# Kernel optimization log

Hardware: AMD Instinct MI355X
Metric: run time of the kernel (lower is better)

The kernel has to match this reference:

```python
import jax, jax.numpy as jnp
import numpy as np

N = 8000          # num_nodes
DEG = 8           # avg out-degree of random road graph
B = 32            # batch size
INPUT_DIM = 2
UNITS = 64        # rnn_units
K = 2             # max_diffusion_step
NUM_SUPPORTS = 2  # dual_random_walk


def _spmm(rows, cols, vals, x):
    # sparse @ dense: y[r] += vals * x[c] for each coo entry (r, c)
    return jax.ops.segment_sum(vals[:, None] * x[cols], rows, num_segments=N)


def _gconv(inputs, state, supports, W, b):
    # Chebyshev-style diffusion conv, faithful to GCONV.forward layout
    Bsz = inputs.shape[0]
    x = jnp.concatenate([inputs.reshape(Bsz, N, -1), state.reshape(Bsz, N, -1)], axis=2)
    F = x.shape[2]                                   # input_dim + units
    x0 = jnp.transpose(x, (1, 2, 0)).reshape(N, F * Bsz)
    xs = [x0]
    for rows, cols, vals in supports:
        x1 = _spmm(rows, cols, vals, x0)
        xs.append(x1)
        xk2, xk1 = x0, x1
        for _ in range(2, K + 1):
            x2 = 2.0 * _spmm(rows, cols, vals, xk1) - xk2
            xs.append(x2)
            xk2, xk1 = xk1, x2
    M = len(xs)                                      # num_matrices = 2*K+1
    xc = jnp.stack(xs).reshape(M, N, F, Bsz)
    xc = jnp.transpose(xc, (3, 1, 2, 0)).reshape(Bsz * N, F * M)
    out = xc @ W + b
    return out.reshape(Bsz, N * W.shape[1])


def setup_inputs() -> dict:
    rng = np.random.default_rng(0)
    rows = np.repeat(np.arange(N, dtype=np.int32), DEG)
    cols = rng.integers(0, N, size=N * DEG).astype(np.int32)
    vals = rng.uniform(0.5, 1.5, size=N * DEG).astype(np.float32)
    # random-walk normalization: rw(A) = D^-1 A ; supports are rw(A).T and rw(A.T).T
    rsum = np.zeros(N, np.float32); np.add.at(rsum, rows, vals)
    csum = np.zeros(N, np.float32); np.add.at(csum, cols, vals)
    rinv = np.where(rsum > 0, 1.0 / np.maximum(rsum, 1e-12), 0.0).astype(np.float32)
    cinv = np.where(csum > 0, 1.0 / np.maximum(csum, 1e-12), 0.0).astype(np.float32)
    # support0 = (D^-1 A)^T: entry (cols[i], rows[i]) = vals[i] * rinv[rows[i]]
    s0_rows, s0_cols, s0_vals = cols, rows, (vals * rinv[rows]).astype(np.float32)
    # support1 = (D_T^-1 A^T)^T: entry (rows[i], cols[i]) = vals[i] * cinv[cols[i]]
    s1_rows, s1_cols, s1_vals = rows, cols, (vals * cinv[cols]).astype(np.float32)

    key = jax.random.key(0)
    k1, k2, k3, k4 = jax.random.split(key, 4)
    F = INPUT_DIM + UNITS
    M = NUM_SUPPORTS * K + 1
    xavier = lambda k, shape: jax.random.normal(k, shape, jnp.float32) * np.float32(np.sqrt(2.0 / (shape[0] + shape[1])))
    W_ru = xavier(k1, (F * M, 2 * UNITS))
    b_ru = jnp.ones((2 * UNITS,), jnp.float32)    # bias_start=1.0
    W_c = xavier(k2, (F * M, UNITS))
    b_c = jnp.zeros((UNITS,), jnp.float32)        # bias_start=0.0
    inputs = jax.random.normal(k3, (B, N * INPUT_DIM), jnp.float32)
    hx = jax.random.normal(k4, (B, N * UNITS), jnp.float32)
    return {
        "inputs": inputs, "hx": hx,
        "W_ru": W_ru, "b_ru": b_ru, "W_c": W_c, "b_c": b_c,
        "s0_rows": jnp.asarray(s0_rows), "s0_cols": jnp.asarray(s0_cols), "s0_vals": jnp.asarray(s0_vals),
        "s1_rows": jnp.asarray(s1_rows), "s1_cols": jnp.asarray(s1_cols), "s1_vals": jnp.asarray(s1_vals),
    }


def reference(inputs, hx, W_ru, b_ru, W_c, b_c,
              s0_rows, s0_cols, s0_vals, s1_rows, s1_cols, s1_vals):
    supports = [(s0_rows, s0_cols, s0_vals), (s1_rows, s1_cols, s1_vals)]
    value = jax.nn.sigmoid(_gconv(inputs, hx, supports, W_ru, b_ru))
    value = value.reshape(-1, N, 2 * UNITS)
    r = value[..., :UNITS].reshape(-1, N * UNITS)
    u = value[..., UNITS:].reshape(-1, N * UNITS)
    c = jnp.tanh(_gconv(inputs, r * hx, supports, W_c, b_c))
    return u * hx + (1.0 - u) * c
```

## Files before the change

### kernel.cpp

```cpp
#include <hip/hip_runtime.h>
#include <stdint.h>

typedef unsigned short u16;
typedef unsigned int   u32;

typedef __attribute__((ext_vector_type(8))) short bf16x8;
typedef __attribute__((ext_vector_type(4))) float f32x4;

#define NNODES 8000
#define BSZ    32
#define UNITS  64
#define EDG    64000
#define ROWCH  288
#define ROWU16 2304
#define KLIN   480
#define HXROW  512000
#define INROW  16000
#define NROW   18432000
#define NSTEPS 15

__device__ __forceinline__ u32 f2bf(float f){
    u32 u = __float_as_uint(f);
    return (u + 0x7FFFu + ((u >> 16) & 1u)) >> 16;
}
__device__ __forceinline__ float bfu(u16 s){ return __uint_as_float(((u32)s) << 16); }
__device__ __forceinline__ float lo16(u32 u){ return __uint_as_float(u << 16); }
__device__ __forceinline__ float hi16(u32 u){ return __uint_as_float(u & 0xFFFF0000u); }
__device__ __forceinline__ float sigm(float x){ return 1.f / (1.f + __expf(-x)); }

#define GLDS(gsrc, ldst) \
    __builtin_amdgcn_global_load_lds((const __attribute__((address_space(1))) void*)(gsrc), \
                                     (__attribute__((address_space(3))) void*)(ldst), 16, 0, 0)

__global__ void hist_k(const int* __restrict__ rows, int* __restrict__ counts){
    int e = blockIdx.x * 256 + threadIdx.x;
    if (e < EDG) atomicAdd(&counts[rows[e]], 1);
}

__global__ __launch_bounds__(256) void scan_k(const int* __restrict__ counts,
                                              int* __restrict__ row_ptr,
                                              int* __restrict__ cursor){
    __shared__ int part[256];
    int t = threadIdx.x;
    int s = 0;
    for (int i = 0; i < 32; ++i){ int r = t*32 + i; if (r < NNODES) s += counts[r]; }
    part[t] = s;
    __syncthreads();
    if (t == 0){
        int run = 0;
        for (int i = 0; i < 256; ++i){ int v = part[i]; part[i] = run; run += v; }
    }
    __syncthreads();
    int run = part[t];
    for (int i = 0; i < 32; ++i){
        int r = t*32 + i;
        if (r < NNODES){ row_ptr[r] = run; cursor[r] = run; run += counts[r]; }
    }
    if (t == 255) row_ptr[NNODES] = run;
}

__global__ void scatter_k(const int* __restrict__ rows, const int* __restrict__ cols,
                          const float* __restrict__ vals, int* __restrict__ cursor,
                          int* __restrict__ cs, float* __restrict__ vs){
    int e = blockIdx.x * 256 + threadIdx.x;
    if (e < EDG){
        int r = rows[e];
        int slot = atomicAdd(&cursor[r], 1);
        cs[slot] = cols[e];
        vs[slot] = vals[e];
    }
}

__global__ void prep_w_k(const float* __restrict__ W_ru, const float* __restrict__ W_c,
                         u16* __restrict__ Wt_ru, u16* __restrict__ Wt_c){
    int id = blockIdx.x * 256 + threadIdx.x;
    if (id < 128*KLIN){
        int j = id & 7;
        int cell = id >> 3;
        int col = cell & 127;
        int sq = cell >> 7;
        int kl = sq*8 + j;
        int m = kl / 96, fp = kl - m*96;
        u16 v = 0;
        if (fp < 66){
            float w;
            if (m == 0)      w = W_ru[(fp*5 + 0)*128 + col] - W_ru[(fp*5 + 2)*128 + col] - W_ru[(fp*5 + 4)*128 + col];
            else if (m == 2) w = 2.f * W_ru[(fp*5 + 2)*128 + col];
            else if (m == 4) w = 2.f * W_ru[(fp*5 + 4)*128 + col];
            else             w = W_ru[(fp*5 + m)*128 + col];
            v = (u16)f2bf(w);
        }
        Wt_ru[id] = v;
    }
    int id2 = id - 128*KLIN;
    if (id2 >= 0 && id2 < 64*KLIN){
        int j = id2 & 7;
        int cell = id2 >> 3;
        int col = cell & 63;
        int sq = cell >> 6;
        int kl = sq*8 + j;
        int m = kl / 96, fp = kl - m*96;
        u16 v = 0;
        if (fp < 66){
            float w;
            if (m == 0)      w = W_c[(fp*5 + 0)*64 + col] - W_c[(fp*5 + 2)*64 + col] - W_c[(fp*5 + 4)*64 + col];
            else if (m == 2) w = 2.f * W_c[(fp*5 + 2)*64 + col];
            else if (m == 4) w = 2.f * W_c[(fp*5 + 4)*64 + col];
            else             w = W_c[(fp*5 + m)*64 + col];
            v = (u16)f2bf(w);
        }
        Wt_c[id2] = v;
    }
}

__global__ __launch_bounds__(256) void build_x0_k(const float* __restrict__ inputs,
                                                  const float* __restrict__ hx,
                                                  u16* __restrict__ X0){
    __shared__ float sl[32*72];
    int n = blockIdx.x, t = threadIdx.x;
    #pragma unroll
    for (int i = 0; i < 8; ++i){
        int idx = t + i*256;
        int b = idx >> 6, f = idx & 63;
        sl[b*72 + 2 + f] = hx[b*HXROW + n*64 + f];
    }
    if (t < 64){
        int b = t >> 1, d = t & 1;
        sl[b*72 + d] = inputs[b*INROW + n*2 + d];
    }
    if (t < 192){
        int b = t / 6, k = t - b*6;
        sl[b*72 + 66 + k] = 0.f;
    }
    __syncthreads();
    #pragma unroll
    for (int i = 0; i < 2; ++i){
        int j = t + i*256;
        if (j < ROWCH){
            int b = j & 31, s = j >> 5;
            const float* p = &sl[b*72 + s*8];
            uint4 o;
            o.x = f2bf(p[0]) | (f2bf(p[1]) << 16);
            o.y = f2bf(p[2]) | (f2bf(p[3]) << 16);
            o.z = f2bf(p[4]) | (f2bf(p[5]) << 16);
            o.w = f2bf(p[6]) | (f2bf(p[7]) << 16);
            ((uint4*)X0)[n*ROWCH + j] = o;
        }
    }
}

__device__ __forceinline__ void acc8(float* a, uint4 q, float v){
    a[0] += v*lo16(q.x); a[1] += v*hi16(q.x);
    a[2] += v*lo16(q.y); a[3] += v*hi16(q.y);
    a[4] += v*lo16(q.z); a[5] += v*hi16(q.z);
    a[6] += v*lo16(q.w); a[7] += v*hi16(q.w);
}
__device__ __forceinline__ uint4 pack8(const float* a){
    uint4 o;
    o.x = f2bf(a[0]) | (f2bf(a[1]) << 16);
    o.y = f2bf(a[2]) | (f2bf(a[3]) << 16);
    o.z = f2bf(a[4]) | (f2bf(a[5]) << 16);
    o.w = f2bf(a[6]) | (f2bf(a[7]) << 16);
    return o;
}

__global__ __launch_bounds__(288) void diff1_k(const u16* __restrict__ X0,
                                               u16* __restrict__ X1a, u16* __restrict__ X1b,
                                               const int* __restrict__ rp,
                                               const int* __restrict__ c0, const float* __restrict__ v0,
                                               const int* __restrict__ c1, const float* __restrict__ v1){
    int t = threadIdx.x;
    if (t >= ROWCH) return;
    int n = blockIdx.x;
    const uint4* xb = (const uint4*)X0;
    float a[8] = {0,0,0,0,0,0,0,0};
    float d[8] = {0,0,0,0,0,0,0,0};
    {
        uint4 q[8]; float vv[8];
        #pragma unroll
        for (int i = 0; i < 8; ++i){
            int c = c1[n*8 + i]; vv[i] = v1[n*8 + i];
            q[i] = xb[(size_t)c*ROWCH + t];
        }
        #pragma unroll
        for (int i = 0; i < 8; ++i) acc8(d, q[i], vv[i]);
    }
    int e = rp[n], end = rp[n+1];
    for (; e + 8 <= end; e += 8){
        uint4 q[8]; float vv[8];
        #pragma unroll
        for (int i = 0; i < 8; ++i){
            int c = c0[e+i]; vv[i] = v0[e+i];
            q[i] = xb[(size_t)c*ROWCH + t];
        }
        #pragma unroll
        for (int i = 0; i < 8; ++i) acc8(a, q[i], vv[i]);
    }
    for (; e < end; ++e){
        int c = c0[e]; float v = v0[e];
        acc8(a, xb[(size_t)c*ROWCH + t], v);
    }
    ((uint4*)X1a)[(size_t)n*ROWCH + t] = pack8(a);
    ((uint4*)X1b)[(size_t)n*ROWCH + t] = pack8(d);
}

__global__ __launch_bounds__(288) void diff2_k(const u16* __restrict__ X1a, const u16* __restrict__ X1b,
                                               u16* __restrict__ Y2a, u16* __restrict__ Y2b,
                                               const int* __restrict__ rp,
                                               const int* __restrict__ c0, const float* __restrict__ v0,
                                               const int* __restrict__ c1, const float* __restrict__ v1){
    int t = threadIdx.x;
    if (t >= ROWCH) return;
    int n = blockIdx.x;
    const uint4* xa = (const uint4*)X1a;
    const uint4* xbb = (const uint4*)X1b;
    float a[8] = {0,0,0,0,0,0,0,0};
    float d[8] = {0,0,0,0,0,0,0,0};
    {
        uint4 q[8]; float vv[8];
        #pragma unroll
        for (int i = 0; i < 8; ++i){
            int c = c1[n*8 + i]; vv[i] = v1[n*8 + i];
            q[i] = xbb[(size_t)c*ROWCH + t];
        }
        #pragma unroll
        for (int i = 0; i < 8; ++i) acc8(d, q[i], vv[i]);
    }
    int e = rp[n], end = rp[n+1];
    for (; e + 8 <= end; e += 8){
        uint4 q[8]; float vv[8];
        #pragma unroll
        for (int i = 0; i < 8; ++i){
            int c = c0[e+i]; vv[i] = v0[e+i];
            q[i] = xa[(size_t)c*ROWCH + t];
        }
        #pragma unroll
        for (int i = 0; i < 8; ++i) acc8(a, q[i], vv[i]);
    }
    for (; e < end; ++e){
        int c = c0[e]; float v = v0[e];
        acc8(a, xa[(size_t)c*ROWCH + t], v);
    }
    ((uint4*)Y2a)[(size_t)n*ROWCH + t] = pack8(a);
    ((uint4*)Y2b)[(size_t)n*ROWCH + t] = pack8(d);
}

__global__ __launch_bounds__(512) void gemm_ru_k(
        const u16* X0, const u16* __restrict__ X1a, const u16* __restrict__ X2a,
        const u16* __restrict__ X1b, const u16* __restrict__ X2b,
        const u16* __restrict__ WtS,
        const float* __restrict__ b_ru,
        u16* __restrict__ U, u16* X0st){
    __shared__ u16 Bs[2][4096];
    const int t = threadIdx.x;
    const int lane = t & 63, w = t >> 6;
    const int node = blockIdx.x*8 + w;
    const int cIn = lane & 15, q = lane >> 4;
    const size_t noff = (size_t)node * ROWU16;

    const u16* xp[5] = { X0 + noff, X1a + noff, X2a + noff, X1b + noff, X2b + noff };

    f32x4 acc[2][8];
    const f32x4 z4 = {0.f,0.f,0.f,0.f};
    #pragma unroll
    for (int rt = 0; rt < 2; ++rt)
        #pragma unroll
        for (int ct = 0; ct < 8; ++ct) acc[rt][ct] = z4;

    GLDS(WtS + t*8, &Bs[0][w*512]);
    bf16x8 A0 = *(const bf16x8*)&xp[0][(size_t)(q*32 + cIn)*8];
    bf16x8 A1 = *(const bf16x8*)&xp[0][(size_t)(q*32 + 16 + cIn)*8];
    __syncthreads();

    int cur = 0;
    #pragma unroll
    for (int st = 0; st < NSTEPS; ++st){
        bf16x8 p0, p1;
        if (st + 1 < NSTEPS){
            GLDS(WtS + (size_t)(st+1)*4096 + t*8, &Bs[cur^1][w*512]);
            const int m2 = (st+1)/3, s2 = (st+1) - m2*3;
            p0 = *(const bf16x8*)&xp[m2][(size_t)((s2*4 + q)*32 + cIn)*8];
            p1 = *(const bf16x8*)&xp[m2][(size_t)((s2*4 + q)*32 + 16 + cIn)*8];
        }
        bf16x8 cb[8];
        #pragma unroll
        for (int ct = 0; ct < 8; ++ct)
            cb[ct] = *(const bf16x8*)&Bs[cur][(q*128 + ct*16 + cIn)*8];
        #pragma unroll
        for (int ct = 0; ct < 8; ++ct){
            acc[0][ct] = __builtin_amdgcn_mfma_f32_16x16x32_bf16(A0, cb[ct], acc[0][ct], 0,0,0);
            acc[1][ct] = __builtin_amdgcn_mfma_f32_16x16x32_bf16(A1, cb[ct], acc[1][ct], 0,0,0);
        }
        __syncthreads();
        if (st + 1 < NSTEPS){ A0 = p0; A1 = p1; }
        cur ^= 1;
    }

    #pragma unroll
    for (int ct = 0; ct < 8; ++ct){
        int col = ct*16 + cIn;
        float bias = b_ru[col];
        #pragma unroll
        for (int rt = 0; rt < 2; ++rt){
            int b0 = rt*16 + q*4;
            f32x4 d = acc[rt][ct];
            if (ct < 4){
                int fp = 2 + col;
                int s = fp >> 3, off = fp & 7;
                #pragma unroll
                for (int i = 0; i < 4; ++i){
                    size_t idx = noff + (size_t)(s*32 + b0 + i)*8 + off;
                    float h = bfu(X0st[idx]);
                    float rg = sigm(d[i] + bias);
                    X0st[idx] = (u16)f2bf(rg * h);
                }
            } else {
                uint2 pk;
                float v0 = sigm(d[0] + bias), v1 = sigm(d[1] + bias);
                float v2 = sigm(d[2] + bias), v3 = sigm(d[3] + bias);
                pk.x = f2bf(v0) | (f2bf(v1) << 16);
                pk.y = f2bf(v2) | (f2bf(v3) << 16);
                *(uint2*)&U[(size_t)node*2048 + (col - 64)*32 + b0] = pk;
            }
        }
    }
}

__global__ __launch_bounds__(512) void gemm_c_k(
        const u16* __restrict__ X0, const u16* __restrict__ X1a, const u16* __restrict__ X2a,
        const u16* __restrict__ X1b, const u16* __restrict__ X2b,
        const u16* __restrict__ WtS,
        const float* __restrict__ b_c, const float* __restrict__ hx,
        const u16* __restrict__ U, float* __restrict__ out){
    __shared__ u16 Bs[2][2048];
    const int t = threadIdx.x;
    const int lane = t & 63, w = t >> 6;
    const int node = blockIdx.x*8 + w;
    const int cIn = lane & 15, q = lane >> 4;
    const size_t noff = (size_t)node * ROWU16;

    const u16* xp[5] = { X0 + noff, X1a + noff, X2a + noff, X1b + noff, X2b + noff };

    f32x4 acc[2][4];
    const f32x4 z4 = {0.f,0.f,0.f,0.f};
    #pragma unroll
    for (int rt = 0; rt < 2; ++rt)
        #pragma unroll
        for (int ct = 0; ct < 4; ++ct) acc[rt][ct] = z4;

    if (t < 256) GLDS(WtS + t*8, &Bs[0][w*512]);
    bf16x8 A0 = *(const bf16x8*)&xp[0][(size_t)(q*32 + cIn)*8];
    bf16x8 A1 = *(const bf16x8*)&xp[0][(size_t)(q*32 + 16 + cIn)*8];
    __syncthreads();

    int cur = 0;
    #pragma unroll
    for (int st = 0; st < NSTEPS; ++st){
        bf16x8 p0, p1;
        if (st + 1 < NSTEPS){
            if (t < 256) GLDS(WtS + (size_t)(st+1)*2048 + t*8, &Bs[cur^1][w*512]);
            const int m2 = (st+1)/3, s2 = (st+1) - m2*3;
            p0 = *(const bf16x8*)&xp[m2][(size_t)((s2*4 + q)*32 + cIn)*8];
            p1 = *(const bf16x8*)&xp[m2][(size_t)((s2*4 + q)*32 + 16 + cIn)*8];
        }
        bf16x8 cb[4];
        #pragma unroll
        for (int ct = 0; ct < 4; ++ct)
            cb[ct] = *(const bf16x8*)&Bs[cur][(q*64 + ct*16 + cIn)*8];
        #pragma unroll
        for (int ct = 0; ct < 4; ++ct){
            acc[0][ct] = __builtin_amdgcn_mfma_f32_16x16x32_bf16(A0, cb[ct], acc[0][ct], 0,0,0);
            acc[1][ct] = __builtin_amdgcn_mfma_f32_16x16x32_bf16(A1, cb[ct], acc[1][ct], 0,0,0);
        }
        __syncthreads();
        if (st + 1 < NSTEPS){ A0 = p0; A1 = p1; }
        cur ^= 1;
    }

    #pragma unroll
    for (int ct = 0; ct < 4; ++ct){
        int col = ct*16 + cIn;
        float bias = b_c[col];
        #pragma unroll
        for (int rt = 0; rt < 2; ++rt){
            int b0 = rt*16 + q*4;
            f32x4 d = acc[rt][ct];
            uint2 up = *(const uint2*)&U[(size_t)node*2048 + col*32 + b0];
            float uu[4] = { lo16(up.x), hi16(up.x), lo16(up.y), hi16(up.y) };
            #pragma unroll
            for (int i = 0; i < 4; ++i){
                float c = tanhf(d[i] + bias);
                size_t gi = (size_t)(b0 + i)*HXROW + node*64 + col;
                float h = hx[gi];
                out[gi] = uu[i]*h + (1.f - uu[i])*c;
            }
        }
    }
}

extern "C" void kernel_launch(void* const* d_in, const int* in_sizes, int n_in,
                              void* d_out, int out_size, void* d_ws, size_t ws_size,
                              hipStream_t stream){
    const float* inputs = (const float*)d_in[0];
    const float* hx     = (const float*)d_in[1];
    const float* W_ru   = (const float*)d_in[2];
    const float* b_ru   = (const float*)d_in[3];
    const float* W_c    = (const float*)d_in[4];
    const float* b_c    = (const float*)d_in[5];
    const int*   s0r    = (const int*)d_in[6];
    const int*   s0c    = (const int*)d_in[7];
    const float* s0v    = (const float*)d_in[8];
    const int*   s1c    = (const int*)d_in[10];
    const float* s1v    = (const float*)d_in[11];
    float* out = (float*)d_out;

    char* ws = (char*)d_ws;
    size_t off = 0;
    auto alloc = [&](size_t bytes) -> char* {
        char* p = ws + off;
        off += (bytes + 255) & ~(size_t)255;
        return p;
    };
    const size_t XBYTES = (size_t)NROW*2 + 2048;
    u16* X0   = (u16*)alloc(XBYTES);
    u16* X1a  = (u16*)alloc(XBYTES);
    u16* X2a  = (u16*)alloc(XBYTES);
    u16* X1b  = (u16*)alloc(XBYTES);
    u16* X2b  = (u16*)alloc(XBYTES);
    u16* U    = (u16*)alloc((size_t)NNODES*2048*2);
    u16* WtRU = (u16*)alloc((size_t)128*KLIN*2);
    u16* WtC  = (u16*)alloc((size_t)64*KLIN*2);
    int* counts  = (int*)alloc((size_t)NNODES*4);
    int* row_ptr = (int*)alloc((size_t)(NNODES+1)*4);
    int* cursor  = (int*)alloc((size_t)NNODES*4);
    int*   cols_s = (int*)alloc((size_t)EDG*4);
    float* vals_s = (float*)alloc((size_t)EDG*4);
    (void)ws_size; (void)in_sizes; (void)n_in; (void)out_size;

    hipMemsetAsync(counts, 0, (size_t)NNODES*4, stream);
    hist_k<<<250, 256, 0, stream>>>(s0r, counts);
    scan_k<<<1, 256, 0, stream>>>(counts, row_ptr, cursor);
    scatter_k<<<250, 256, 0, stream>>>(s0r, s0c, s0v, cursor, cols_s, vals_s);

    prep_w_k<<<360, 256, 0, stream>>>(W_ru, W_c, WtRU, WtC);
    build_x0_k<<<NNODES, 256, 0, stream>>>(inputs, hx, X0);

    diff1_k<<<NNODES, 288, 0, stream>>>(X0, X1a, X1b, row_ptr, cols_s, vals_s, s1c, s1v);
    diff2_k<<<NNODES, 288, 0, stream>>>(X1a, X1b, X2a, X2b, row_ptr, cols_s, vals_s, s1c, s1v);

    gemm_ru_k<<<NNODES/8, 512, 0, stream>>>(X0, X1a, X2a, X1b, X2b, WtRU, b_ru, U, X0);

    diff1_k<<<NNODES, 288, 0, stream>>>(X0, X1a, X1b, row_ptr, cols_s, vals_s, s1c, s1v);
    diff2_k<<<NNODES, 288, 0, stream>>>(X1a, X1b, X2a, X2b, row_ptr, cols_s, vals_s, s1c, s1v);

    gemm_c_k<<<NNODES/8, 512, 0, stream>>>(X0, X1a, X2a, X1b, X2b, WtC, b_c, hx, U, out);
}
```

Before: 665.4 us.

## Interleave diffusion matrices per node and shrink padded GEMM K dimension

The five separate diffusion buffers (X0, X1a, X2a, X1b, X2b) are merged into one node-major buffer where each node's five 288-chunk blocks sit next to each other. The GEMM K layout changes from 96-wide padded slots per matrix to 72-wide, cutting K from 480 to 384 and the number of pipeline steps from 15 to 12. The intent is to reduce wasted MFMA work on zero padding and make each wave's A-operand reads contiguous per node. The cost is a larger stride between nodes for the gathers in the diffusion kernels, which may lower locality there, and an extra memset of the padding tail.

Result: no change. 664.8 us (-0.1%).

```diff
diff --git a/kernel.cpp b/kernel.cpp
--- a/kernel.cpp
+++ b/kernel.cpp
@@ -12,12 +12,12 @@
 #define UNITS  64
 #define EDG    64000
 #define ROWCH  288
-#define ROWU16 2304
-#define KLIN   480
+#define NODECH 1440
+#define NODEU16 11520
+#define KLIN   384
+#define NSTEPS 12
 #define HXROW  512000
 #define INROW  16000
-#define NROW   18432000
-#define NSTEPS 15
 
 __device__ __forceinline__ u32 f2bf(float f){
     u32 u = __float_as_uint(f);
@@ -80,9 +80,9 @@
         int col = cell & 127;
         int sq = cell >> 7;
         int kl = sq*8 + j;
-        int m = kl / 96, fp = kl - m*96;
+        int m = kl / 72, fp = kl - m*72;
         u16 v = 0;
-        if (fp < 66){
+        if (m < 5 && fp < 66){
             float w;
             if (m == 0)      w = W_ru[(fp*5 + 0)*128 + col] - W_ru[(fp*5 + 2)*128 + col] - W_ru[(fp*5 + 4)*128 + col];
             else if (m == 2) w = 2.f * W_ru[(fp*5 + 2)*128 + col];
@@ -99,9 +99,9 @@
         int col = cell & 63;
         int sq = cell >> 6;
         int kl = sq*8 + j;
-        int m = kl / 96, fp = kl - m*96;
+        int m = kl / 72, fp = kl - m*72;
         u16 v = 0;
-        if (fp < 66){
+        if (m < 5 && fp < 66){
             float w;
             if (m == 0)      w = W_c[(fp*5 + 0)*64 + col] - W_c[(fp*5 + 2)*64 + col] - W_c[(fp*5 + 4)*64 + col];
             else if (m == 2) w = 2.f * W_c[(fp*5 + 2)*64 + col];
@@ -115,7 +115,7 @@
 
 __global__ __launch_bounds__(256) void build_x0_k(const float* __restrict__ inputs,
                                                   const float* __restrict__ hx,
-                                                  u16* __restrict__ X0){
+                                                  u16* __restrict__ Xu){
     __shared__ float sl[32*72];
     int n = blockIdx.x, t = threadIdx.x;
     #pragma unroll
@@ -144,7 +144,7 @@
             o.y = f2bf(p[2]) | (f2bf(p[3]) << 16);
             o.z = f2bf(p[4]) | (f2bf(p[5]) << 16);
             o.w = f2bf(p[6]) | (f2bf(p[7]) << 16);
-            ((uint4*)X0)[n*ROWCH + j] = o;
+            ((uint4*)Xu)[(size_t)n*NODECH + j] = o;
         }
     }
 }
@@ -164,15 +164,14 @@
     return o;
 }
 
-__global__ __launch_bounds__(288) void diff1_k(const u16* __restrict__ X0,
-                                               u16* __restrict__ X1a, u16* __restrict__ X1b,
+__global__ __launch_bounds__(288) void diff1_k(u16* __restrict__ Xu,
                                                const int* __restrict__ rp,
                                                const int* __restrict__ c0, const float* __restrict__ v0,
                                                const int* __restrict__ c1, const float* __restrict__ v1){
     int t = threadIdx.x;
     if (t >= ROWCH) return;
     int n = blockIdx.x;
-    const uint4* xb = (const uint4*)X0;
+    const uint4* xb = (const uint4*)Xu;
     float a[8] = {0,0,0,0,0,0,0,0};
     float d[8] = {0,0,0,0,0,0,0,0};
     {
@@ -180,7 +179,7 @@
         #pragma unroll
         for (int i = 0; i < 8; ++i){
             int c = c1[n*8 + i]; vv[i] = v1[n*8 + i];
-            q[i] = xb[(size_t)c*ROWCH + t];
+            q[i] = xb[(size_t)c*NODECH + t];
         }
         #pragma unroll
         for (int i = 0; i < 8; ++i) acc8(d, q[i], vv[i]);
@@ -191,29 +190,27 @@
         #pragma unroll
         for (int i = 0; i < 8; ++i){
             int c = c0[e+i]; vv[i] = v0[e+i];
-            q[i] = xb[(size_t)c*ROWCH + t];
+            q[i] = xb[(size_t)c*NODECH + t];
         }
         #pragma unroll
         for (int i = 0; i < 8; ++i) acc8(a, q[i], vv[i]);
     }
     for (; e < end; ++e){
         int c = c0[e]; float v = v0[e];
-        acc8(a, xb[(size_t)c*ROWCH + t], v);
-    }
-    ((uint4*)X1a)[(size_t)n*ROWCH + t] = pack8(a);
-    ((uint4*)X1b)[(size_t)n*ROWCH + t] = pack8(d);
-}
-
-__global__ __launch_bounds__(288) void diff2_k(const u16* __restrict__ X1a, const u16* __restrict__ X1b,
-                                               u16* __restrict__ Y2a, u16* __restrict__ Y2b,
+        acc8(a, xb[(size_t)c*NODECH + t], v);
+    }
+    ((uint4*)Xu)[(size_t)n*NODECH + 1*ROWCH + t] = pack8(a);
+    ((uint4*)Xu)[(size_t)n*NODECH + 3*ROWCH + t] = pack8(d);
+}
+
+__global__ __launch_bounds__(288) void diff2_k(u16* __restrict__ Xu,
                                                const int* __restrict__ rp,
                                                const int* __restrict__ c0, const float* __restrict__ v0,
                                                const int* __restrict__ c1, const float* __restrict__ v1){
     int t = threadIdx.x;
     if (t >= ROWCH) return;
     int n = blockIdx.x;
-    const uint4* xa = (const uint4*)X1a;
-    const uint4* xbb = (const uint4*)X1b;
+    const uint4* xb = (const uint4*)Xu;
     float a[8] = {0,0,0,0,0,0,0,0};
     float d[8] = {0,0,0,0,0,0,0,0};
     {
@@ -221,7 +218,7 @@
         #pragma unroll
         for (int i = 0; i < 8; ++i){
             int c = c1[n*8 + i]; vv[i] = v1[n*8 + i];
-            q[i] = xbb[(size_t)c*ROWCH + t];
+            q[i] = xb[(size_t)c*NODECH + 3*ROWCH + t];
         }
         #pragma unroll
         for (int i = 0; i < 8; ++i) acc8(d, q[i], vv[i]);
@@ -232,22 +229,21 @@
         #pragma unroll
         for (int i = 0; i < 8; ++i){
             int c = c0[e+i]; vv[i] = v0[e+i];
-            q[i] = xa[(size_t)c*ROWCH + t];
+            q[i] = xb[(size_t)c*NODECH + 1*ROWCH + t];
         }
         #pragma unroll
         for (int i = 0; i < 8; ++i) acc8(a, q[i], vv[i]);
     }
     for (; e < end; ++e){
         int c = c0[e]; float v = v0[e];
-        acc8(a, xa[(size_t)c*ROWCH + t], v);
-    }
-    ((uint4*)Y2a)[(size_t)n*ROWCH + t] = pack8(a);
-    ((uint4*)Y2b)[(size_t)n*ROWCH + t] = pack8(d);
+        acc8(a, xb[(size_t)c*NODECH + 1*ROWCH + t], v);
+    }
+    ((uint4*)Xu)[(size_t)n*NODECH + 2*ROWCH + t] = pack8(a);
+    ((uint4*)Xu)[(size_t)n*NODECH + 4*ROWCH + t] = pack8(d);
 }
 
 __global__ __launch_bounds__(512) void gemm_ru_k(
-        const u16* X0, const u16* __restrict__ X1a, const u16* __restrict__ X2a,
-        const u16* __restrict__ X1b, const u16* __restrict__ X2b,
+        const u16* Xu,
         const u16* __restrict__ WtS,
         const float* __restrict__ b_ru,
         u16* __restrict__ U, u16* X0st){
@@ -256,9 +252,8 @@
     const int lane = t & 63, w = t >> 6;
     const int node = blockIdx.x*8 + w;
     const int cIn = lane & 15, q = lane >> 4;
-    const size_t noff = (size_t)node * ROWU16;
-
-    const u16* xp[5] = { X0 + noff, X1a + noff, X2a + noff, X1b + noff, X2b + noff };
+    const size_t noff = (size_t)node * NODEU16;
+    const u16* Xn = Xu + noff;
 
     f32x4 acc[2][8];
     const f32x4 z4 = {0.f,0.f,0.f,0.f};
@@ -268,8 +263,8 @@
         for (int ct = 0; ct < 8; ++ct) acc[rt][ct] = z4;
 
     GLDS(WtS + t*8, &Bs[0][w*512]);
-    bf16x8 A0 = *(const bf16x8*)&xp[0][(size_t)(q*32 + cIn)*8];
-    bf16x8 A1 = *(const bf16x8*)&xp[0][(size_t)(q*32 + 16 + cIn)*8];
+    bf16x8 A0 = *(const bf16x8*)&Xn[(size_t)(q*32 + cIn)*8];
+    bf16x8 A1 = *(const bf16x8*)&Xn[(size_t)(q*32 + 16 + cIn)*8];
     __syncthreads();
 
     int cur = 0;
@@ -278,9 +273,8 @@
         bf16x8 p0, p1;
         if (st + 1 < NSTEPS){
             GLDS(WtS + (size_t)(st+1)*4096 + t*8, &Bs[cur^1][w*512]);
-            const int m2 = (st+1)/3, s2 = (st+1) - m2*3;
-            p0 = *(const bf16x8*)&xp[m2][(size_t)((s2*4 + q)*32 + cIn)*8];
-            p1 = *(const bf16x8*)&xp[m2][(size_t)((s2*4 + q)*32 + 16 + cIn)*8];
+            p0 = *(const bf16x8*)&Xn[(size_t)(((st+1)*4 + q)*32 + cIn)*8];
+            p1 = *(const bf16x8*)&Xn[(size_t)(((st+1)*4 + q)*32 + 16 + cIn)*8];
         }
         bf16x8 cb[8];
         #pragma unroll
@@ -327,8 +321,7 @@
 }
 
 __global__ __launch_bounds__(512) void gemm_c_k(
-        const u16* __restrict__ X0, const u16* __restrict__ X1a, const u16* __restrict__ X2a,
-        const u16* __restrict__ X1b, const u16* __restrict__ X2b,
+        const u16* __restrict__ Xu,
         const u16* __restrict__ WtS,
         const float* __restrict__ b_c, const float* __restrict__ hx,
         const u16* __restrict__ U, float* __restrict__ out){
@@ -337,9 +330,8 @@
     const int lane = t & 63, w = t >> 6;
     const int node = blockIdx.x*8 + w;
     const int cIn = lane & 15, q = lane >> 4;
-    const size_t noff = (size_t)node * ROWU16;
-
-    const u16* xp[5] = { X0 + noff, X1a + noff, X2a + noff, X1b + noff, X2b + noff };
+    const size_t noff = (size_t)node * NODEU16;
+    const u16* Xn = Xu + noff;
 
     f32x4 acc[2][4];
     const f32x4 z4 = {0.f,0.f,0.f,0.f};
@@ -349,8 +341,8 @@
         for (int ct = 0; ct < 4; ++ct) acc[rt][ct] = z4;
 
     if (t < 256) GLDS(WtS + t*8, &Bs[0][w*512]);
-    bf16x8 A0 = *(const bf16x8*)&xp[0][(size_t)(q*32 + cIn)*8];
-    bf16x8 A1 = *(const bf16x8*)&xp[0][(size_t)(q*32 + 16 + cIn)*8];
+    bf16x8 A0 = *(const bf16x8*)&Xn[(size_t)(q*32 + cIn)*8];
+    bf16x8 A1 = *(const bf16x8*)&Xn[(size_t)(q*32 + 16 + cIn)*8];
     __syncthreads();
 
     int cur = 0;
@@ -359,9 +351,8 @@
         bf16x8 p0, p1;
         if (st + 1 < NSTEPS){
             if (t < 256) GLDS(WtS + (size_t)(st+1)*2048 + t*8, &Bs[cur^1][w*512]);
-            const int m2 = (st+1)/3, s2 = (st+1) - m2*3;
-            p0 = *(const bf16x8*)&xp[m2][(size_t)((s2*4 + q)*32 + cIn)*8];
-            p1 = *(const bf16x8*)&xp[m2][(size_t)((s2*4 + q)*32 + 16 + cIn)*8];
+            p0 = *(const bf16x8*)&Xn[(size_t)(((st+1)*4 + q)*32 + cIn)*8];
+            p1 = *(const bf16x8*)&Xn[(size_t)(((st+1)*4 + q)*32 + 16 + cIn)*8];
         }
         bf16x8 cb[4];
         #pragma unroll
@@ -421,12 +412,8 @@
         off += (bytes + 255) & ~(size_t)255;
         return p;
     };
-    const size_t XBYTES = (size_t)NROW*2 + 2048;
-    u16* X0   = (u16*)alloc(XBYTES);
-    u16* X1a  = (u16*)alloc(XBYTES);
-    u16* X2a  = (u16*)alloc(XBYTES);
-    u16* X1b  = (u16*)alloc(XBYTES);
-    u16* X2b  = (u16*)alloc(XBYTES);
+    const size_t XU_BYTES = (size_t)NNODES * NODEU16 * 2;
+    u16* Xu   = (u16*)alloc(XU_BYTES + 4096);
     u16* U    = (u16*)alloc((size_t)NNODES*2048*2);
     u16* WtRU = (u16*)alloc((size_t)128*KLIN*2);
     u16* WtC  = (u16*)alloc((size_t)64*KLIN*2);
@@ -438,20 +425,21 @@
     (void)ws_size; (void)in_sizes; (void)n_in; (void)out_size;
 
     hipMemsetAsync(counts, 0, (size_t)NNODES*4, stream);
+    hipMemsetAsync((char*)Xu + XU_BYTES, 0, 4096, stream);
     hist_k<<<250, 256, 0, stream>>>(s0r, counts);
     scan_k<<<1, 256, 0, stream>>>(counts, row_ptr, cursor);
     scatter_k<<<250, 256, 0, stream>>>(s0r, s0c, s0v, cursor, cols_s, vals_s);
 
-    prep_w_k<<<360, 256, 0, stream>>>(W_ru, W_c, WtRU, WtC);
-    build_x0_k<<<NNODES, 256, 0, stream>>>(inputs, hx, X0);
-
-    diff1_k<<<NNODES, 288, 0, stream>>>(X0, X1a, X1b, row_ptr, cols_s, vals_s, s1c, s1v);
-    diff2_k<<<NNODES, 288, 0, stream>>>(X1a, X1b, X2a, X2b, row_ptr, cols_s, vals_s, s1c, s1v);
-
-    gemm_ru_k<<<NNODES/8, 512, 0, stream>>>(X0, X1a, X2a, X1b, X2b, WtRU, b_ru, U, X0);
-
-    diff1_k<<<NNODES, 288, 0, stream>>>(X0, X1a, X1b, row_ptr, cols_s, vals_s, s1c, s1v);
-    diff2_k<<<NNODES, 288, 0, stream>>>(X1a, X1b, X2a, X2b, row_ptr, cols_s, vals_s, s1c, s1v);
-
-    gemm_c_k<<<NNODES/8, 512, 0, stream>>>(X0, X1a, X2a, X1b, X2b, WtC, b_c, hx, U, out);
-}
+    prep_w_k<<<288, 256, 0, stream>>>(W_ru, W_c, WtRU, WtC);
+    build_x0_k<<<NNODES, 256, 0, stream>>>(inputs, hx, Xu);
+
+    diff1_k<<<NNODES, 288, 0, stream>>>(Xu, row_ptr, cols_s, vals_s, s1c, s1v);
+    diff2_k<<<NNODES, 288, 0, stream>>>(Xu, row_ptr, cols_s, vals_s, s1c, s1v);
+
+    gemm_ru_k<<<NNODES/8, 512, 0, stream>>>(Xu, WtRU, b_ru, U, Xu);
+
+    diff1_k<<<NNODES, 288, 0, stream>>>(Xu, row_ptr, cols_s, vals_s, s1c, s1v);
+    diff2_k<<<NNODES, 288, 0, stream>>>(Xu, row_ptr, cols_s, vals_s, s1c, s1v);
+
+    gemm_c_k<<<NNODES/8, 512, 0, stream>>>(Xu, WtC, b_c, hx, U, out);
+}
```
